# Performance work log

Hardware: AMD Instinct MI355X
Metric: run time of the kernel (lower is better)

Reference implementation:

```python
import jax, jax.numpy as jnp
import numpy as np

L = 8            # hash grid levels
T = 2 ** 19      # table size per level
F = 4            # feature dims per level
H = 64           # hidden features
BASE_RES, MAX_RES = 16.0, 1024.0
RES = jnp.asarray(BASE_RES * (MAX_RES / BASE_RES) ** (np.arange(L) / (L - 1)), dtype=jnp.float32)
PRIMES = jnp.array([1, 2654435761, 805459861], dtype=jnp.uint32)
CORNERS = jnp.array([[i >> 2 & 1, i >> 1 & 1, i & 1] for i in range(8)], dtype=jnp.float32)  # [8,3]
CORNERS_U = CORNERS.astype(jnp.uint32)


def hash_grid_encode(points, tables):
    # points: [N,3] in [0,1]; tables: [L,T,F] -> [N, L*F]
    def level(table, res):
        p = points * res                       # [N,3]
        p0 = jnp.floor(p)
        frac = p - p0                          # [N,3]
        idx0 = p0.astype(jnp.uint32)
        cidx = idx0[:, None, :] + CORNERS_U[None]          # [N,8,3]
        h = cidx * PRIMES                                   # uint32 wraparound
        h = (h[..., 0] ^ h[..., 1] ^ h[..., 2]) % jnp.uint32(T)
        feats = table[h.astype(jnp.int32)]                  # [N,8,F]
        w = jnp.prod(jnp.where(CORNERS[None] == 1.0, frac[:, None, :], 1.0 - frac[:, None, :]), axis=-1)  # [N,8]
        return jnp.sum(feats * w[..., None], axis=1)        # [N,F]
    out = jax.vmap(level, in_axes=(0, 0))(tables, RES)      # [L,N,F]
    return jnp.transpose(out, (1, 0, 2)).reshape(points.shape[0], L * F)


def sh4_encode(d):
    # 4th order (16-component) spherical harmonics of unit directions
    d = d / jnp.linalg.norm(d, axis=-1, keepdims=True)
    x, y, z = d[..., 0], d[..., 1], d[..., 2]
    xx, yy, zz = x * x, y * y, z * z
    return jnp.stack([
        jnp.full_like(x, 0.28209479177387814),
        -0.48860251190291987 * y,
        0.48860251190291987 * z,
        -0.48860251190291987 * x,
        1.0925484305920792 * x * y,
        -1.0925484305920792 * y * z,
        0.94617469575755997 * zz - 0.31539156525252005,
        -1.0925484305920792 * x * z,
        0.54627421529603959 * (xx - yy),
        -0.59004358992664352 * y * (3.0 * xx - yy),
        2.8906114426405538 * x * y * z,
        -0.45704579946446572 * y * (4.0 * zz - xx - yy),
        0.37317633259011546 * z * (2.0 * zz - 3.0 * xx - 3.0 * yy),
        -0.45704579946446572 * x * (4.0 * zz - xx - yy),
        1.4453057213202769 * z * (xx - yy),
        -0.59004358992664352 * x * (xx - 3.0 * yy),
    ], axis=-1)


def _dense(key, fan_in, fan_out):
    kw, kb = jax.random.split(key)
    W = jax.random.normal(kw, (fan_in, fan_out), jnp.float32) / jnp.sqrt(fan_in)
    b = jnp.zeros((fan_out,), jnp.float32)
    return W, b


def setup_inputs() -> dict:
    key = jax.random.key(0)
    ks = jax.random.split(key, 10)
    N = 524288
    input_points = jax.random.uniform(ks[0], (N, 3), jnp.float32)
    input_views = jax.random.normal(ks[1], (N, 3), jnp.float32)
    tables = jax.random.uniform(ks[2], (L, T, F), jnp.float32, -1e-4, 1e-4)
    W1, b1 = _dense(ks[3], L * F, H)
    W2, b2 = _dense(ks[4], H, H)
    W3, b3 = _dense(ks[5], H, 16)
    W4, b4 = _dense(ks[6], 15 + 16, H)
    W5, b5 = _dense(ks[7], H, H)
    W6, b6 = _dense(ks[8], H, H)
    W7, b7 = _dense(ks[9], H, 3)
    return dict(input_points=input_points, input_views=input_views, tables=tables,
                W1=W1, b1=b1, W2=W2, b2=b2, W3=W3, b3=b3, W4=W4, b4=b4,
                W5=W5, b5=b5, W6=W6, b6=b6, W7=W7, b7=b7)


def reference(input_points, input_views, tables, W1, b1, W2, b2, W3, b3, W4, b4, W5, b5, W6, b6, W7, b7):
    enc = hash_grid_encode(input_points, tables)       # [N,32]
    x = jax.nn.relu(enc @ W1 + b1)
    x = jax.nn.relu(x @ W2 + b2)
    x = x @ W3 + b3                                    # [N,16]
    densities = jax.nn.relu(x[..., 0])
    enc_dir = sh4_encode(input_views)                  # [N,16]
    x = jnp.concatenate([x[..., 1:], enc_dir], axis=-1)  # [N,31]
    x = jax.nn.relu(x @ W4 + b4)
    x = jax.nn.relu(x @ W5 + b5)
    x = jax.nn.relu(x @ W6 + b6)
    x = x @ W7 + b7                                    # [N,3]
    colors = jax.nn.sigmoid(x)
    return colors, densities
```

## Files before the change

### kernel.cpp

```cpp
#include <hip/hip_runtime.h>
#include <math.h>

#define TSZ (1u << 19)

typedef __attribute__((ext_vector_type(8))) short bf8_t;
typedef __attribute__((ext_vector_type(4))) float f32x4;

struct ResArr { float r[8]; };
struct WPtrs { const float* w[7]; };

__device__ __forceinline__ unsigned short f2b(float x) {
    unsigned u = __float_as_uint(x);
    return (unsigned short)((u + 0x7fffu + ((u >> 16) & 1u)) >> 16);
}
__device__ __forceinline__ unsigned pack2(float a, float b) {
    return (unsigned)f2b(a) | ((unsigned)f2b(b) << 16);
}

__device__ __forceinline__ int swadr(int row, int e) {
    return row * 128 + ((((e >> 3) ^ (row & 7)) << 4)) + ((e & 7) << 1);
}

__device__ __forceinline__ float dec8(unsigned b) {
    unsigned bits = ((b & 0x80u) << 24) | (((b & 0x7fu) << 20) + 0x35800000u);
    return __uint_as_float(bits);
}

__device__ __forceinline__ unsigned enc8(float x) {
    float v = x * 1048576.0f;
    unsigned u = __float_as_uint(v);
    unsigned s = (u >> 24) & 0x80u;
    unsigned ua = u & 0x7fffffffu;
    unsigned r = ua + 0x7ffffu + ((ua >> 20) & 1u);
    int E = (int)(r >> 23) - 120;
    unsigned nrm = ((unsigned)E << 3) | ((r >> 20) & 7u);
    float t = __uint_as_float(ua) * 512.0f + 12582912.0f;
    unsigned den = __float_as_uint(t) & 0xfu;
    unsigned mag = (__uint_as_float(ua) >= 0.015625f) ? nrm : den;
    return s | mag;
}

__global__ void prep_tables(const float4* __restrict__ tbl, uint4* __restrict__ out, int n4) {
    int i = blockIdx.x * 256 + threadIdx.x;
    if (i >= n4) return;
    uint4 o;
    {
        float4 v = tbl[4 * i + 0];
        o.x = enc8(v.x) | (enc8(v.y) << 8) | (enc8(v.z) << 16) | (enc8(v.w) << 24);
    }
    {
        float4 v = tbl[4 * i + 1];
        o.y = enc8(v.x) | (enc8(v.y) << 8) | (enc8(v.z) << 16) | (enc8(v.w) << 24);
    }
    {
        float4 v = tbl[4 * i + 2];
        o.z = enc8(v.x) | (enc8(v.y) << 8) | (enc8(v.z) << 16) | (enc8(v.w) << 24);
    }
    {
        float4 v = tbl[4 * i + 3];
        o.w = enc8(v.x) | (enc8(v.y) << 8) | (enc8(v.z) << 16) | (enc8(v.w) << 24);
    }
    out[i] = o;
}

__global__ void prep_weights(WPtrs wp, unsigned short* __restrict__ out) {
    int idx = blockIdx.x * 256 + threadIdx.x;
    if (idx >= 18432) return;
    int layer, base;
    if      (idx < 2048)  { layer = 0; base = 0;     }
    else if (idx < 6144)  { layer = 1; base = 2048;  }
    else if (idx < 7168)  { layer = 2; base = 6144;  }
    else if (idx < 9216)  { layer = 3; base = 7168;  }
    else if (idx < 13312) { layer = 4; base = 9216;  }
    else if (idx < 17408) { layer = 5; base = 13312; }
    else                  { layer = 6; base = 17408; }
    int rel  = idx - base;
    int frag = rel >> 9;
    int r    = rel & 511;
    int lane = r >> 3, j = r & 7;
    int quad = lane >> 4, col16 = lane & 15;
    int KS = (layer == 0 || layer == 3) ? 1 : 2;
    int nt = frag / KS, ks = frag % KS;
    int k = ks * 32 + quad * 8 + j;
    int n = nt * 16 + col16;
    int Kreal = (layer == 0) ? 32 : (layer == 3) ? 31 : 64;
    int Nw    = (layer == 2) ? 16 : (layer == 6) ? 3  : 64;
    float v = 0.0f;
    if (k < Kreal && n < Nw) v = wp.w[layer][k * Nw + n];
    out[idx] = f2b(v);
}

__global__ void __launch_bounds__(256, 2) ngp_mfma(
    const float* __restrict__ pts, const float* __restrict__ views,
    const unsigned* __restrict__ tab8,
    const unsigned short* __restrict__ wfrag,
    const float* __restrict__ b1, const float* __restrict__ b2,
    const float* __restrict__ b3, const float* __restrict__ b4,
    const float* __restrict__ b5, const float* __restrict__ b6,
    const float* __restrict__ b7,
    ResArr res, float* __restrict__ out_col, float* __restrict__ out_den,
    int npts)
{
    __shared__ unsigned char act[4][8192];
    const int tid   = threadIdx.x;
    const int w     = tid >> 6;
    const int lane  = tid & 63;
    const int quad  = lane >> 4;
    const int col16 = lane & 15;
    unsigned char* actb = act[w];

    const int n0 = blockIdx.x * 256 + w * 64;
    if (n0 >= npts) return;
    int pt = n0 + lane;
    int ptc = pt < npts ? pt : npts - 1;

    const float px = pts[3 * ptc + 0];
    const float py = pts[3 * ptc + 1];
    const float pz = pts[3 * ptc + 2];
    float vx = views[3 * ptc + 0], vy = views[3 * ptc + 1], vz = views[3 * ptc + 2];

    unsigned gv[8][8];
    float tfr[8][3];
#pragma unroll
    for (int l = 0; l < 8; ++l) {
        float rr = res.r[l];
        float fx = px * rr, fy = py * rr, fz = pz * rr;
        float f0x = floorf(fx), f0y = floorf(fy), f0z = floorf(fz);
        unsigned ix = (unsigned)f0x, iy = (unsigned)f0y, iz = (unsigned)f0z;
        tfr[l][0] = fx - f0x; tfr[l][1] = fy - f0y; tfr[l][2] = fz - f0z;
        unsigned hy  = iy * 2654435761u,  hz  = iz * 805459861u;
        unsigned hy1 = hy + 2654435761u,  hz1 = hz + 805459861u;
        const unsigned* tl = tab8 + (size_t)l * TSZ;
#pragma unroll
        for (int c = 0; c < 8; ++c) {
            unsigned h = (ix + ((c >> 2) & 1u)) ^ ((c & 2) ? hy1 : hy) ^ ((c & 1) ? hz1 : hz);
            gv[l][c] = tl[h & (TSZ - 1u)];
        }
    }
    float4 stash;
#pragma unroll
    for (int l = 0; l < 8; ++l) {
        float tx = tfr[l][0], ty = tfr[l][1], tz = tfr[l][2];
        float4 a = make_float4(0.f, 0.f, 0.f, 0.f);
#pragma unroll
        for (int c = 0; c < 8; ++c) {
            float wt = ((c & 4) ? tx : 1.0f - tx) *
                       ((c & 2) ? ty : 1.0f - ty) *
                       ((c & 1) ? tz : 1.0f - tz);
            unsigned u = gv[l][c];
            a.x = fmaf(wt, dec8(u & 255u), a.x);
            a.y = fmaf(wt, dec8((u >> 8) & 255u), a.y);
            a.z = fmaf(wt, dec8((u >> 16) & 255u), a.z);
            a.w = fmaf(wt, dec8(u >> 24), a.w);
        }
        if ((l & 1) == 0) {
            stash = a;
        } else {
            uint4 pk;
            pk.x = pack2(stash.x, stash.y);
            pk.y = pack2(stash.z, stash.w);
            pk.z = pack2(a.x, a.y);
            pk.w = pack2(a.z, a.w);
            *(uint4*)(actb + lane * 128 + ((((l >> 1)) ^ (lane & 7)) << 4)) = pk;
        }
    }

    float inv = rsqrtf(vx * vx + vy * vy + vz * vz);
    vx *= inv; vy *= inv; vz *= inv;
    float xx = vx * vx, yy = vy * vy, zz = vz * vz;
    float sh[16];
    sh[0]  = 0.28209479177387814f;
    sh[1]  = -0.48860251190291987f * vy;
    sh[2]  = 0.48860251190291987f * vz;
    sh[3]  = -0.48860251190291987f * vx;
    sh[4]  = 1.0925484305920792f * vx * vy;
    sh[5]  = -1.0925484305920792f * vy * vz;
    sh[6]  = 0.94617469575755997f * zz - 0.31539156525252005f;
    sh[7]  = -1.0925484305920792f * vx * vz;
    sh[8]  = 0.54627421529603959f * (xx - yy);
    sh[9]  = -0.59004358992664352f * vy * (3.0f * xx - yy);
    sh[10] = 2.8906114426405538f * vx * vy * vz;
    sh[11] = -0.45704579946446572f * vy * (4.0f * zz - xx - yy);
    sh[12] = 0.37317633259011546f * vz * (2.0f * zz - 3.0f * xx - 3.0f * yy);
    sh[13] = -0.45704579946446572f * vx * (4.0f * zz - xx - yy);
    sh[14] = 1.4453057213202769f * vz * (xx - yy);
    sh[15] = -0.59004358992664352f * vx * (xx - 3.0f * yy);

#define LAYER_STD(KS, FB, BIAS)                                                          \
    {                                                                                    \
        bf8_t A[4][KS];                                                                  \
        _Pragma("unroll") for (int mt = 0; mt < 4; ++mt)                                 \
            _Pragma("unroll") for (int ks = 0; ks < KS; ++ks)                            \
                A[mt][ks] = *(const bf8_t*)(actb + swadr(mt * 16 + col16, ks * 32 + quad * 8)); \
        _Pragma("unroll") for (int nt = 0; nt < 4; ++nt) {                               \
            float bv = BIAS[nt * 16 + col16];                                            \
            f32x4 acc[4];                                                                \
            _Pragma("unroll") for (int mt = 0; mt < 4; ++mt) acc[mt] = f32x4{bv, bv, bv, bv}; \
            _Pragma("unroll") for (int ks = 0; ks < KS; ++ks) {                          \
                bf8_t B = ((const bf8_t*)(wfrag + FB + (nt * KS + ks) * 512))[lane];     \
                _Pragma("unroll") for (int mt = 0; mt < 4; ++mt)                         \
                    acc[mt] = __builtin_amdgcn_mfma_f32_16x16x32_bf16(A[mt][ks], B, acc[mt], 0, 0, 0); \
            }                                                                            \
            _Pragma("unroll") for (int mt = 0; mt < 4; ++mt)                             \
                _Pragma("unroll") for (int r = 0; r < 4; ++r) {                          \
                    int row = mt * 16 + quad * 4 + r;                                    \
                    *(unsigned short*)(actb + swadr(row, nt * 16 + col16)) =             \
                        f2b(fmaxf(acc[mt][r], 0.0f));                                    \
                }                                                                        \
        }                                                                                \
    }

    LAYER_STD(1, 0, b1)
    LAYER_STD(2, 2048, b2)

    {
        bf8_t A[4][2];
#pragma unroll
        for (int mt = 0; mt < 4; ++mt)
#pragma unroll
            for (int ks = 0; ks < 2; ++ks)
                A[mt][ks] = *(const bf8_t*)(actb + swadr(mt * 16 + col16, ks * 32 + quad * 8));
        float bv = b3[col16];
        f32x4 acc[4];
#pragma unroll
        for (int mt = 0; mt < 4; ++mt) acc[mt] = f32x4{bv, bv, bv, bv};
#pragma unroll
        for (int ks = 0; ks < 2; ++ks) {
            bf8_t B = ((const bf8_t*)(wfrag + 6144 + ks * 512))[lane];
#pragma unroll
            for (int mt = 0; mt < 4; ++mt)
                acc[mt] = __builtin_amdgcn_mfma_f32_16x16x32_bf16(A[mt][ks], B, acc[mt], 0, 0, 0);
        }
#pragma unroll
        for (int mt = 0; mt < 4; ++mt)
#pragma unroll
            for (int r = 0; r < 4; ++r) {
                int row = mt * 16 + quad * 4 + r;
                float v = acc[mt][r];
                if (col16 == 0) {
                    if (n0 + row < npts) out_den[n0 + row] = fmaxf(v, 0.0f);
                } else {
                    *(unsigned short*)(actb + swadr(row, col16 - 1)) = f2b(v);
                }
            }
    }

#pragma unroll
    for (int i = 0; i < 16; ++i)
        *(unsigned short*)(actb + swadr(lane, 15 + i)) = f2b(sh[i]);
    *(unsigned short*)(actb + swadr(lane, 31)) = 0;

    LAYER_STD(1, 7168, b4)
    LAYER_STD(2, 9216, b5)
    LAYER_STD(2, 13312, b6)

    {
        bf8_t A[4][2];
#pragma unroll
        for (int mt = 0; mt < 4; ++mt)
#pragma unroll
            for (int ks = 0; ks < 2; ++ks)
                A[mt][ks] = *(const bf8_t*)(actb + swadr(mt * 16 + col16, ks * 32 + quad * 8));
        float bv = (col16 < 3) ? b7[col16] : 0.0f;
        f32x4 acc[4];
#pragma unroll
        for (int mt = 0; mt < 4; ++mt) acc[mt] = f32x4{bv, bv, bv, bv};
#pragma unroll
        for (int ks = 0; ks < 2; ++ks) {
            bf8_t B = ((const bf8_t*)(wfrag + 17408 + ks * 512))[lane];
#pragma unroll
            for (int mt = 0; mt < 4; ++mt)
                acc[mt] = __builtin_amdgcn_mfma_f32_16x16x32_bf16(A[mt][ks], B, acc[mt], 0, 0, 0);
        }
        if (col16 < 3) {
#pragma unroll
            for (int mt = 0; mt < 4; ++mt)
#pragma unroll
                for (int r = 0; r < 4; ++r) {
                    int row = mt * 16 + quad * 4 + r;
                    if (n0 + row < npts) {
                        float s = 1.0f / (1.0f + expf(-acc[mt][r]));
                        out_col[(size_t)(n0 + row) * 3 + col16] = s;
                    }
                }
        }
    }
#undef LAYER_STD
}

extern "C" void kernel_launch(void* const* d_in, const int* in_sizes, int n_in,
                              void* d_out, int out_size, void* d_ws, size_t ws_size,
                              hipStream_t stream) {
    const float* pts    = (const float*)d_in[0];
    const float* views  = (const float*)d_in[1];
    const float* tables = (const float*)d_in[2];
    const float* W1 = (const float*)d_in[3];  const float* b1 = (const float*)d_in[4];
    const float* W2 = (const float*)d_in[5];  const float* b2 = (const float*)d_in[6];
    const float* W3 = (const float*)d_in[7];  const float* b3 = (const float*)d_in[8];
    const float* W4 = (const float*)d_in[9];  const float* b4 = (const float*)d_in[10];
    const float* W5 = (const float*)d_in[11]; const float* b5 = (const float*)d_in[12];
    const float* W6 = (const float*)d_in[13]; const float* b6 = (const float*)d_in[14];
    const float* W7 = (const float*)d_in[15]; const float* b7 = (const float*)d_in[16];

    const int N = in_sizes[0] / 3;
    float* out = (float*)d_out;
    float* out_col = out;
    float* out_den = out + (size_t)3 * N;

    unsigned* tab8        = (unsigned*)d_ws;
    unsigned short* wfrag = (unsigned short*)((char*)d_ws + (size_t)(TSZ) * 8 * 4);

    const int n4 = 8 * TSZ / 4;
    prep_tables<<<(n4 + 255) / 256, 256, 0, stream>>>((const float4*)tables, (uint4*)tab8, n4);

    WPtrs wp;
    wp.w[0] = W1; wp.w[1] = W2; wp.w[2] = W3; wp.w[3] = W4;
    wp.w[4] = W5; wp.w[5] = W6; wp.w[6] = W7;
    prep_weights<<<(18432 + 255) / 256, 256, 0, stream>>>(wp, wfrag);

    ResArr res;
    for (int l = 0; l < 8; ++l)
        res.r[l] = (float)(16.0 * pow(64.0, (double)l / 7.0));

    const int grid = (N + 255) / 256;
    ngp_mfma<<<grid, 256, 0, stream>>>(pts, views, tab8, wfrag,
                                       b1, b2, b3, b4, b5, b6, b7,
                                       res, out_col, out_den, N);
}
```

Measured before the change: 307.9 us.

## Decode fp8 table entries into packed fp16 and interpolate with half2 FMAs

The trilinear interpolation now decodes each custom 8-bit feature into fp16 bit patterns with byte permutes and accumulates with packed half2 FMAs, scaling back to fp32 once per level. This replaces four scalar fp32 FMAs per corner and cuts ALU work. The corner weights are factored, with yz products computed once per level. The table and weight prep kernels are merged into one launch to remove a kernel launch. The risk is lost precision from accumulating in fp16, including possible subnormal handling issues.

```diff
diff --git a/kernel.cpp b/kernel.cpp
--- a/kernel.cpp
+++ b/kernel.cpp
@@ -5,6 +5,7 @@
 
 typedef __attribute__((ext_vector_type(8))) short bf8_t;
 typedef __attribute__((ext_vector_type(4))) float f32x4;
+typedef _Float16 h2_t __attribute__((ext_vector_type(2)));
 
 struct ResArr { float r[8]; };
 struct WPtrs { const float* w[7]; };
@@ -19,11 +20,6 @@
 
 __device__ __forceinline__ int swadr(int row, int e) {
     return row * 128 + ((((e >> 3) ^ (row & 7)) << 4)) + ((e & 7) << 1);
-}
-
-__device__ __forceinline__ float dec8(unsigned b) {
-    unsigned bits = ((b & 0x80u) << 24) | (((b & 0x7fu) << 20) + 0x35800000u);
-    return __uint_as_float(bits);
 }
 
 __device__ __forceinline__ unsigned enc8(float x) {
@@ -40,31 +36,20 @@
     return s | mag;
 }
 
-__global__ void prep_tables(const float4* __restrict__ tbl, uint4* __restrict__ out, int n4) {
-    int i = blockIdx.x * 256 + threadIdx.x;
-    if (i >= n4) return;
-    uint4 o;
-    {
-        float4 v = tbl[4 * i + 0];
-        o.x = enc8(v.x) | (enc8(v.y) << 8) | (enc8(v.z) << 16) | (enc8(v.w) << 24);
-    }
-    {
-        float4 v = tbl[4 * i + 1];
-        o.y = enc8(v.x) | (enc8(v.y) << 8) | (enc8(v.z) << 16) | (enc8(v.w) << 24);
-    }
-    {
-        float4 v = tbl[4 * i + 2];
-        o.z = enc8(v.x) | (enc8(v.y) << 8) | (enc8(v.z) << 16) | (enc8(v.w) << 24);
-    }
-    {
-        float4 v = tbl[4 * i + 3];
-        o.w = enc8(v.x) | (enc8(v.y) << 8) | (enc8(v.z) << 16) | (enc8(v.w) << 24);
-    }
-    out[i] = o;
-}
-
-__global__ void prep_weights(WPtrs wp, unsigned short* __restrict__ out) {
-    int idx = blockIdx.x * 256 + threadIdx.x;
+__global__ void prep_all(const float4* __restrict__ tbl, uint4* __restrict__ tab_out,
+                         WPtrs wp, unsigned short* __restrict__ wfrag) {
+    int b = blockIdx.x;
+    if (b < 4096) {
+        int i = b * 256 + threadIdx.x;
+        uint4 o;
+        { float4 v = tbl[4 * i + 0]; o.x = enc8(v.x) | (enc8(v.y) << 8) | (enc8(v.z) << 16) | (enc8(v.w) << 24); }
+        { float4 v = tbl[4 * i + 1]; o.y = enc8(v.x) | (enc8(v.y) << 8) | (enc8(v.z) << 16) | (enc8(v.w) << 24); }
+        { float4 v = tbl[4 * i + 2]; o.z = enc8(v.x) | (enc8(v.y) << 8) | (enc8(v.z) << 16) | (enc8(v.w) << 24); }
+        { float4 v = tbl[4 * i + 3]; o.w = enc8(v.x) | (enc8(v.y) << 8) | (enc8(v.z) << 16) | (enc8(v.w) << 24); }
+        tab_out[i] = o;
+        return;
+    }
+    int idx = (b - 4096) * 256 + threadIdx.x;
     if (idx >= 18432) return;
     int layer, base;
     if      (idx < 2048)  { layer = 0; base = 0;     }
@@ -87,7 +72,7 @@
     int Nw    = (layer == 2) ? 16 : (layer == 6) ? 3  : 64;
     float v = 0.0f;
     if (k < Kreal && n < Nw) v = wp.w[layer][k * Nw + n];
-    out[idx] = f2b(v);
+    wfrag[idx] = f2b(v);
 }
 
 __global__ void __launch_bounds__(256, 2) ngp_mfma(
@@ -141,26 +126,36 @@
 #pragma unroll
     for (int l = 0; l < 8; ++l) {
         float tx = tfr[l][0], ty = tfr[l][1], tz = tfr[l][2];
-        float4 a = make_float4(0.f, 0.f, 0.f, 0.f);
+        float wx1 = tx, wx0 = 1.0f - tx;
+        float wy1 = ty, wy0 = 1.0f - ty;
+        float wz1 = tz, wz0 = 1.0f - tz;
+        float wyz[4] = { wy0 * wz0, wy0 * wz1, wy1 * wz0, wy1 * wz1 };
+        h2_t acc01 = { (_Float16)0, (_Float16)0 };
+        h2_t acc23 = { (_Float16)0, (_Float16)0 };
 #pragma unroll
         for (int c = 0; c < 8; ++c) {
-            float wt = ((c & 4) ? tx : 1.0f - tx) *
-                       ((c & 2) ? ty : 1.0f - ty) *
-                       ((c & 1) ? tz : 1.0f - tz);
+            float wt = ((c & 4) ? wx1 : wx0) * wyz[c & 3];
+            unsigned ws = (unsigned)__builtin_bit_cast(unsigned short, (_Float16)wt);
+            h2_t w2 = __builtin_bit_cast(h2_t, __builtin_amdgcn_perm(0u, ws, 0x01000100u));
             unsigned u = gv[l][c];
-            a.x = fmaf(wt, dec8(u & 255u), a.x);
-            a.y = fmaf(wt, dec8((u >> 8) & 255u), a.y);
-            a.z = fmaf(wt, dec8((u >> 16) & 255u), a.z);
-            a.w = fmaf(wt, dec8(u >> 24), a.w);
-        }
+            unsigned p01 = __builtin_amdgcn_perm(0u, u, 0x01040004u);
+            unsigned p23 = __builtin_amdgcn_perm(0u, u, 0x03040204u);
+            unsigned m01 = (((p01 >> 1) & 0x3F803F80u) + 0x20002000u) | (p01 & 0x80008000u);
+            unsigned m23 = (((p23 >> 1) & 0x3F803F80u) + 0x20002000u) | (p23 & 0x80008000u);
+            acc01 = __builtin_bit_cast(h2_t, m01) * w2 + acc01;
+            acc23 = __builtin_bit_cast(h2_t, m23) * w2 + acc23;
+        }
+        const float SC = 9.5367431640625e-07f;
+        float a0 = (float)acc01[0] * SC, a1 = (float)acc01[1] * SC;
+        float a2 = (float)acc23[0] * SC, a3 = (float)acc23[1] * SC;
         if ((l & 1) == 0) {
-            stash = a;
+            stash = make_float4(a0, a1, a2, a3);
         } else {
             uint4 pk;
             pk.x = pack2(stash.x, stash.y);
             pk.y = pack2(stash.z, stash.w);
-            pk.z = pack2(a.x, a.y);
-            pk.w = pack2(a.z, a.w);
+            pk.z = pack2(a0, a1);
+            pk.w = pack2(a2, a3);
             *(uint4*)(actb + lane * 128 + ((((l >> 1)) ^ (lane & 7)) << 4)) = pk;
         }
     }
@@ -310,13 +305,10 @@
     unsigned* tab8        = (unsigned*)d_ws;
     unsigned short* wfrag = (unsigned short*)((char*)d_ws + (size_t)(TSZ) * 8 * 4);
 
-    const int n4 = 8 * TSZ / 4;
-    prep_tables<<<(n4 + 255) / 256, 256, 0, stream>>>((const float4*)tables, (uint4*)tab8, n4);
-
     WPtrs wp;
     wp.w[0] = W1; wp.w[1] = W2; wp.w[2] = W3; wp.w[3] = W4;
     wp.w[4] = W5; wp.w[5] = W6; wp.w[6] = W7;
-    prep_weights<<<(18432 + 255) / 256, 256, 0, stream>>>(wp, wfrag);
+    prep_all<<<4096 + 72, 256, 0, stream>>>((const float4*)tables, (uint4*)tab8, wp, wfrag);
 
     ResArr res;
     for (int l = 0; l < 8; ++l)
```

Measured after the change: 309.8 us. Within noise of the previous version (+0.6%).
